# Kernel tuning notes

Measured on AMD Instinct MI355X. Metric: run time of the kernel, lower is better.

## Reference

```python
import jax, jax.numpy as jnp
import numpy as np

EMBED_DIM = 1024
NUM_HEADS = 16
DEPTH = 12
HEAD_DIM = EMBED_DIM // NUM_HEADS // 2  # 32
LAMBDA_INIT = float(0.8 - 0.6 * np.exp(-0.3 * DEPTH))
B, T = 2, 2048


def setup_inputs() -> dict:
    key = jax.random.key(0)
    ks = jax.random.split(key, 10)
    s = 0.02
    return {
        "query": jax.random.normal(ks[0], (B, T, EMBED_DIM), jnp.float32),
        "Wq": jax.random.normal(ks[1], (EMBED_DIM, EMBED_DIM), jnp.float32) * s,
        "Wk": jax.random.normal(ks[2], (EMBED_DIM, EMBED_DIM), jnp.float32) * s,
        "Wv": jax.random.normal(ks[3], (EMBED_DIM, EMBED_DIM), jnp.float32) * s,
        "Wo": jax.random.normal(ks[4], (EMBED_DIM, EMBED_DIM), jnp.float32) * s,
        "lambda_q1": jax.random.normal(ks[5], (HEAD_DIM,), jnp.float32) * 0.1,
        "lambda_k1": jax.random.normal(ks[6], (HEAD_DIM,), jnp.float32) * 0.1,
        "lambda_q2": jax.random.normal(ks[7], (HEAD_DIM,), jnp.float32) * 0.1,
        "lambda_k2": jax.random.normal(ks[8], (HEAD_DIM,), jnp.float32) * 0.1,
        "subln_w": jnp.ones((2 * HEAD_DIM,), jnp.float32),
    }


def reference(query, Wq, Wk, Wv, Wo, lambda_q1, lambda_k1, lambda_q2, lambda_k2, subln_w):
    Bsz, Tt, E = query.shape
    H, hd = NUM_HEADS, HEAD_DIM
    scaling = hd ** -0.5
    # projections (torch Linear: x @ W.T), W stored [out, in]
    q = jnp.einsum('bte,fe->btf', query, Wq).reshape(Bsz, Tt, 2 * H, hd).transpose(0, 2, 1, 3)
    k = jnp.einsum('bse,fe->bsf', query, Wk).reshape(Bsz, Tt, 2 * H, hd).transpose(0, 2, 1, 3)
    v = jnp.einsum('bse,fe->bsf', query, Wv).reshape(Bsz, Tt, H, 2 * hd).transpose(0, 2, 1, 3)
    q = q * scaling
    # dual attention map [B, 2H, T, T], softmax in fp32
    scores = jnp.einsum('bhtd,bhsd->bhts', q, k)
    attn_w = jax.nn.softmax(scores.astype(jnp.float32), axis=-1).astype(q.dtype)
    # learned lambda
    lam1 = jnp.exp(jnp.sum(lambda_q1 * lambda_k1))
    lam2 = jnp.exp(jnp.sum(lambda_q2 * lambda_k2))
    lam = lam1 - lam2 + LAMBDA_INIT
    aw = attn_w.reshape(Bsz, H, 2, Tt, Tt)
    aw = aw[:, :, 0] - lam * aw[:, :, 1]  # [B, H, T, T]
    attn = jnp.einsum('bhts,bhsd->bhtd', aw, v)  # [B, H, T, 2*hd]
    # RMSNorm over last dim (fp32), eps=1e-5, elementwise affine
    x32 = attn.astype(jnp.float32)
    normed = (x32 * jax.lax.rsqrt(jnp.mean(x32 * x32, axis=-1, keepdims=True) + 1e-5)).astype(attn.dtype)
    attn = normed * subln_w
    attn = attn * (1.0 - LAMBDA_INIT)
    out = attn.transpose(0, 2, 1, 3).reshape(Bsz, Tt, H * 2 * hd)
    return jnp.einsum('bte,fe->btf', out, Wo)
```

## Files before the change

### kernel.cpp

```cpp
#include <hip/hip_runtime.h>

typedef short bf16x8 __attribute__((ext_vector_type(8)));
typedef float f32x4 __attribute__((ext_vector_type(4)));
typedef float f32x16 __attribute__((ext_vector_type(16)));
typedef unsigned short ushort_t;
typedef unsigned int uint32;

#define LAMBDA_INIT 0.7836057665316245f
#define TT 2048
#define EE 1024

__device__ __forceinline__ ushort_t f2bf(float x) {
  uint32 b = __float_as_uint(x);
  b += 0x7fffu + ((b >> 16) & 1u);
  return (ushort_t)(b >> 16);
}

__device__ __forceinline__ uint32 cvtpk(float lo, float hi) {
  uint32 r;
  asm("v_cvt_pk_bf16_f32 %0, %1, %2" : "=v"(r) : "v"(lo), "v"(hi));
  return r;
}

__device__ __forceinline__ float fexp2(float x) {
#if __has_builtin(__builtin_amdgcn_exp2f)
  return __builtin_amdgcn_exp2f(x);
#else
  return exp2f(x);
#endif
}

__device__ __forceinline__ bf16x8 mkfrag(uint32 a, uint32 b, uint32 c, uint32 d) {
  union { uint32 w[4]; bf16x8 v; } u;
  u.w[0] = a; u.w[1] = b; u.w[2] = c; u.w[3] = d;
  return u.v;
}

__device__ __forceinline__ void gload16(const void* g, void* l) {
  __builtin_amdgcn_global_load_lds(
      (const __attribute__((address_space(1))) uint32*)g,
      (__attribute__((address_space(3))) uint32*)l, 16, 0, 0);
}

__global__ __launch_bounds__(256) void cvt_all(const float* __restrict__ X,
                                               const float* __restrict__ Wq,
                                               const float* __restrict__ Wk,
                                               const float* __restrict__ Wv,
                                               const float* __restrict__ Wo,
                                               ushort_t* __restrict__ out) {
  const int i = blockIdx.x * 256 + threadIdx.x;
  const float* src;
  int off;
  if (i < 1048576)      { src = X;  off = 0; }
  else if (i < 1310720) { src = Wq; off = 1048576; }
  else if (i < 1572864) { src = Wk; off = 1310720; }
  else if (i < 1835008) { src = Wv; off = 1572864; }
  else                  { src = Wo; off = 1835008; }
  const float4 v = reinterpret_cast<const float4*>(src)[i - off];
  ushort4 o;
  o.x = f2bf(v.x); o.y = f2bf(v.y); o.z = f2bf(v.z); o.w = f2bf(v.w);
  reinterpret_cast<ushort4*>(out)[i] = o;
}

__global__ __launch_bounds__(256) void gemm_bt(const ushort_t* __restrict__ A,
                                               const ushort_t* __restrict__ B,
                                               float* __restrict__ C,
                                               int M, int N, int K, float scale) {
  __shared__ ushort_t As[128 * 32];
  __shared__ ushort_t Bs[128 * 32];
  const int tid = threadIdx.x;
  const int lane = tid & 63, wid = tid >> 6;
  const int wr = wid >> 1, wc = wid & 1;
  const int r16 = lane & 15, g = lane >> 4;
  const int m0 = blockIdx.x * 128, n0 = blockIdx.y * 128;
  f32x4 acc[4][4] = {};
  for (int k0 = 0; k0 < K; k0 += 32) {
#pragma unroll
    for (int c = 0; c < 2; ++c) {
      int eo = wid * 1024 + c * 512 + lane * 8;
      int row = eo >> 5, col = eo & 31;
      gload16(A + (size_t)(m0 + row) * K + k0 + col, As + wid * 1024 + c * 512);
      gload16(B + (size_t)(n0 + row) * K + k0 + col, Bs + wid * 1024 + c * 512);
    }
    __syncthreads();
    bf16x8 af[4], bfg[4];
#pragma unroll
    for (int m = 0; m < 4; ++m)
      af[m] = *reinterpret_cast<const bf16x8*>(As + (wr * 64 + m * 16 + r16) * 32 + g * 8);
#pragma unroll
    for (int n = 0; n < 4; ++n)
      bfg[n] = *reinterpret_cast<const bf16x8*>(Bs + (wc * 64 + n * 16 + r16) * 32 + g * 8);
#pragma unroll
    for (int m = 0; m < 4; ++m)
#pragma unroll
      for (int n = 0; n < 4; ++n)
        acc[m][n] = __builtin_amdgcn_mfma_f32_16x16x32_bf16(af[m], bfg[n], acc[m][n], 0, 0, 0);
    __syncthreads();
  }
#pragma unroll
  for (int m = 0; m < 4; ++m)
#pragma unroll
    for (int n = 0; n < 4; ++n)
#pragma unroll
      for (int r = 0; r < 4; ++r) {
        int row = m0 + wr * 64 + m * 16 + g * 4 + r;
        int col = n0 + wc * 64 + n * 16 + r16;
        C[(size_t)row * N + col] = acc[m][n][r] * scale;
      }
}

#define SHALF(Sbase, Gbase)                                                  \
  do {                                                                       \
    _Pragma("unroll") for (int j_ = 0; j_ < 2; ++j_) {                       \
      const int c_ = wid * 2 + j_;                                           \
      gload16((Gbase) + (size_t)(c_ * 8 + (lane >> 3)) * EE +                \
                  (((lane & 7) ^ (lane >> 3)) << 3),                         \
              (Sbase) + c_ * 512);                                           \
    }                                                                        \
  } while (0)

#define CHUNK(mp)                                                            \
  do {                                                                       \
    __builtin_amdgcn_s_setprio(1);                                           \
    _Pragma("unroll") for (int mm_ = 0; mm_ < 2; ++mm_) {                    \
      const int m_ = (mp) * 2 + mm_;                                         \
      _Pragma("unroll") for (int n_ = 0; n_ < 4; ++n_) {                     \
        acc[m_][n_] = __builtin_amdgcn_mfma_f32_16x16x32_bf16(               \
            af[m_][0], bfr[n_][0], acc[m_][n_], 0, 0, 0);                    \
        acc[m_][n_] = __builtin_amdgcn_mfma_f32_16x16x32_bf16(               \
            af[m_][1], bfr[n_][1], acc[m_][n_], 0, 0, 0);                    \
      }                                                                      \
    }                                                                        \
    __builtin_amdgcn_s_setprio(0);                                           \
  } while (0)

__global__ __launch_bounds__(512, 2) void qkv_gemm256(const ushort_t* __restrict__ A,
                                                      const ushort_t* __restrict__ B,
                                                      ushort_t* __restrict__ C,
                                                      float scale) {
  __shared__ ushort_t Asm[2][16384];
  __shared__ ushort_t Bsm[2][16384];
  const int NKT = EE / 64;
  const int tid = threadIdx.x, lane = tid & 63, wid = tid >> 6;
  const int wr = wid >> 2, wc = wid & 3;
  const int r16 = lane & 15, g = lane >> 4;
  const int w = (blockIdx.x & 7) * 24 + (blockIdx.x >> 3);
  const int bx = w & 15, by = w >> 4;
  const int m0 = bx * 256, n0 = by * 256;
  const ushort_t* Ab = A + (size_t)m0 * EE;
  const ushort_t* Bb = B + (size_t)n0 * EE;

#pragma unroll
  for (int kt = 0; kt < 2; ++kt) {
    SHALF(Asm[kt], Ab + kt * 64);
    SHALF(Asm[kt] + 8192, Ab + (size_t)128 * EE + kt * 64);
    SHALF(Bsm[kt], Bb + kt * 64);
    SHALF(Bsm[kt] + 8192, Bb + (size_t)128 * EE + kt * 64);
  }

  f32x4 acc[8][4] = {};
  for (int t = 0; t < NKT; ++t) {
    const int b = t & 1;
    if (t < NKT - 1) asm volatile("s_waitcnt vmcnt(8)" ::: "memory");
    else             asm volatile("s_waitcnt vmcnt(0)" ::: "memory");
    __builtin_amdgcn_s_barrier();
    asm volatile("" ::: "memory");
    bf16x8 af[8][2], bfr[4][2];
#pragma unroll
    for (int m = 0; m < 8; ++m) {
      const int row = wr * 128 + m * 16 + r16;
#pragma unroll
      for (int kk = 0; kk < 2; ++kk)
        af[m][kk] = *reinterpret_cast<const bf16x8*>(
            Asm[b] + row * 64 + (((kk * 4 + g) ^ (r16 & 7)) << 3));
    }
#pragma unroll
    for (int n = 0; n < 4; ++n) {
      const int row = wc * 64 + n * 16 + r16;
#pragma unroll
      for (int kk = 0; kk < 2; ++kk)
        bfr[n][kk] = *reinterpret_cast<const bf16x8*>(
            Bsm[b] + row * 64 + (((kk * 4 + g) ^ (r16 & 7)) << 3));
    }
    asm volatile("s_waitcnt lgkmcnt(0)" ::: "memory");
    __builtin_amdgcn_s_barrier();
    asm volatile("" ::: "memory");
    const int ts = t + 2;
    const bool st = ts < NKT;
    if (st) SHALF(Asm[b], Ab + ts * 64);
    CHUNK(0);
    if (st) SHALF(Asm[b] + 8192, Ab + (size_t)128 * EE + ts * 64);
    CHUNK(1);
    if (st) SHALF(Bsm[b], Bb + ts * 64);
    CHUNK(2);
    if (st) SHALF(Bsm[b] + 8192, Bb + (size_t)128 * EE + ts * 64);
    CHUNK(3);
  }

  const size_t MN = (size_t)4096 * EE;
#pragma unroll
  for (int m = 0; m < 8; ++m)
#pragma unroll
    for (int n = 0; n < 4; ++n) {
      const int col = n0 + wc * 64 + n * 16 + r16;
      const int seg = col >> 10;
      const int cl = col & 1023;
      if (seg == 2) {
        int row0 = m0 + wr * 128 + m * 16 + g * 4;
        int bb2 = row0 >> 11, t0v = row0 & (TT - 1);
        ushort4 pk;
        pk.x = f2bf(acc[m][n][0]); pk.y = f2bf(acc[m][n][1]);
        pk.z = f2bf(acc[m][n][2]); pk.w = f2bf(acc[m][n][3]);
        *reinterpret_cast<ushort4*>(
            C + 2 * MN + ((size_t)(bb2 * 16 + (cl >> 6)) * 64 + (cl & 63)) * TT + t0v) = pk;
      } else {
        const float sc = (seg == 0) ? scale : 1.0f;
        const size_t base = (size_t)seg * MN;
#pragma unroll
        for (int r = 0; r < 4; ++r) {
          int row = m0 + wr * 128 + m * 16 + g * 4 + r;
          C[base + (size_t)row * EE + cl] = f2bf(acc[m][n][r] * sc);
        }
      }
    }
}

#define PHALF(sv, lacc, oT0, oT1, vf)                                                   \
  do {                                                                                  \
    float p_[16];                                                                       \
    _Pragma("unroll") for (int i_ = 0; i_ < 16; ++i_) p_[i_] = fexp2(sv[i_]);           \
    lacc += (((p_[0] + p_[1]) + (p_[2] + p_[3])) + ((p_[4] + p_[5]) + (p_[6] + p_[7]))) \
          + (((p_[8] + p_[9]) + (p_[10] + p_[11])) +                                    \
             ((p_[12] + p_[13]) + (p_[14] + p_[15])));                                  \
    auto wA_ = __builtin_amdgcn_permlane32_swap((int)cvtpk(p_[0], p_[1]),               \
                                                (int)cvtpk(p_[4], p_[5]), false, false);\
    auto wB_ = __builtin_amdgcn_permlane32_swap((int)cvtpk(p_[2], p_[3]),               \
                                                (int)cvtpk(p_[6], p_[7]), false, false);\
    auto wC_ = __builtin_amdgcn_permlane32_swap((int)cvtpk(p_[8], p_[9]),               \
                                                (int)cvtpk(p_[12], p_[13]), false, false);\
    auto wD_ = __builtin_amdgcn_permlane32_swap((int)cvtpk(p_[10], p_[11]),             \
                                                (int)cvtpk(p_[14], p_[15]), false, false);\
    bf16x8 pa0_ = mkfrag(wA_[0], wB_[0], wA_[1], wB_[1]);                               \
    bf16x8 pa1_ = mkfrag(wC_[0], wD_[0], wC_[1], wD_[1]);                               \
    oT0 = __builtin_amdgcn_mfma_f32_32x32x16_bf16(pa0_, vf[0][0], oT0, 0, 0, 0);        \
    oT0 = __builtin_amdgcn_mfma_f32_32x32x16_bf16(pa1_, vf[1][0], oT0, 0, 0, 0);        \
    oT1 = __builtin_amdgcn_mfma_f32_32x32x16_bf16(pa0_, vf[0][1], oT1, 0, 0, 0);        \
    oT1 = __builtin_amdgcn_mfma_f32_32x32x16_bf16(pa1_, vf[1][1], oT1, 0, 0, 0);        \
  } while (0)

#define STAGE(bi, kv0)                                                                  \
  do {                                                                                  \
    const int r8_ = lane >> 3;                                                          \
    const int g_ = (lane & 7) ^ r8_;                                                    \
    _Pragma("unroll") for (int c2_ = 0; c2_ < 2; ++c2_) {                               \
      const int c_ = wid * 2 + c2_;                                                     \
      gload16(Kg + (size_t)((kv0) + c_ * 8 + r8_) * EE + g_ * 8,                        \
              Ksm[bi] + c_ * 512);                                                      \
      gload16(Vg + (size_t)(c_ * 8 + r8_) * TT + (kv0) + g_ * 8,                        \
              Vsm[bi] + c_ * 512);                                                      \
    }                                                                                   \
  } while (0)

__global__ __launch_bounds__(256, 2) void attn_fused(
    const ushort_t* __restrict__ Q, const ushort_t* __restrict__ K,
    const ushort_t* __restrict__ Vt,
    const float* __restrict__ lq1, const float* __restrict__ lk1,
    const float* __restrict__ lq2, const float* __restrict__ lk2,
    const float* __restrict__ w, ushort_t* __restrict__ X2) {
  __shared__ ushort_t Ksm[2][64 * 64];
  __shared__ ushort_t Vsm[2][64 * 64];
  const int tid = threadIdx.x, lane = tid & 63, wid = tid >> 6;
  const int l31 = lane & 31, hh = lane >> 5;
  const int bid = blockIdx.x;
  const int slice = (bid & 7) + 8 * (bid >> 7);
  const int qb = (bid >> 3) & 15;
  const int bb = slice >> 4, h = slice & 15;
  const int q0 = qb * 128 + wid * 32;

  float prod = (lane < 32) ? lq1[l31] * lk1[l31] : lq2[l31] * lk2[l31];
#pragma unroll
  for (int off = 1; off < 32; off <<= 1) prod += __shfl_xor(prod, off, 32);
  const float lam = __expf(__shfl(prod, 0, 64)) - __expf(__shfl(prod, 32, 64)) + LAMBDA_INIT;

  const ushort_t* Qp = Q + (size_t)(bb * TT + q0 + l31) * EE + h * 64 + hh * 8;
  const bf16x8 qf00 = *reinterpret_cast<const bf16x8*>(Qp);
  const bf16x8 qf01 = *reinterpret_cast<const bf16x8*>(Qp + 16);
  const bf16x8 qf10 = *reinterpret_cast<const bf16x8*>(Qp + 32);
  const bf16x8 qf11 = *reinterpret_cast<const bf16x8*>(Qp + 48);

  const ushort_t* Kg = K + (size_t)bb * TT * EE + h * 64;
  const ushort_t* Vg = Vt + (size_t)(bb * 16 + h) * 64 * TT;
  const int swz = (l31 & 7) << 3;

  f32x16 o00 = {}, o01 = {}, o10 = {}, o11 = {};
  float l0 = 0.f, l1 = 0.f;

  STAGE(0, 0);
  for (int it = 0; it < TT / 64; ++it) {
    const int cur = it & 1;
    __syncthreads();
    if (it + 1 < TT / 64) STAGE(cur ^ 1, (it + 1) * 64);

    const ushort_t* Kt_ = Ksm[cur];
    const ushort_t* Vt_ = Vsm[cur];
#pragma unroll
    for (int s = 0; s < 2; ++s) {
      bf16x8 kf[2][2], vf[2][2];
#pragma unroll
      for (int hf = 0; hf < 2; ++hf)
#pragma unroll
        for (int ks = 0; ks < 2; ++ks)
          kf[hf][ks] = *reinterpret_cast<const bf16x8*>(
              Kt_ + (s * 32 + l31) * 64 + ((hf * 32 + ks * 16 + hh * 8) ^ swz));
#pragma unroll
      for (int ks = 0; ks < 2; ++ks)
#pragma unroll
        for (int dc = 0; dc < 2; ++dc)
          vf[ks][dc] = *reinterpret_cast<const bf16x8*>(
              Vt_ + (dc * 32 + l31) * 64 + ((s * 32 + ks * 16 + hh * 8) ^ swz));

      __builtin_amdgcn_s_setprio(1);
      const f32x16 zz = {};
      f32x16 s0_ = __builtin_amdgcn_mfma_f32_32x32x16_bf16(kf[0][0], qf00, zz, 0, 0, 0);
      s0_ = __builtin_amdgcn_mfma_f32_32x32x16_bf16(kf[0][1], qf01, s0_, 0, 0, 0);
      f32x16 s1_ = __builtin_amdgcn_mfma_f32_32x32x16_bf16(kf[1][0], qf10, zz, 0, 0, 0);
      s1_ = __builtin_amdgcn_mfma_f32_32x32x16_bf16(kf[1][1], qf11, s1_, 0, 0, 0);
      __builtin_amdgcn_s_setprio(0);
      PHALF(s0_, l0, o00, o01, vf);
      PHALF(s1_, l1, o10, o11, vf);
    }
  }

  {
    auto t0 = __builtin_amdgcn_permlane32_swap(__float_as_int(l0), __float_as_int(l0),
                                               false, false);
    l0 = __int_as_float(t0[0]) + __int_as_float(t0[1]);
    auto t1 = __builtin_amdgcn_permlane32_swap(__float_as_int(l1), __float_as_int(l1),
                                               false, false);
    l1 = __int_as_float(t1[0]) + __int_as_float(t1[1]);
  }

  const float w0v = w[l31];
  const float w1v = w[32 + l31];
#pragma unroll
  for (int r = 0; r < 16; ++r) {
    const int qrel = (r & 3) + 8 * (r >> 2) + 4 * hh;
    const float il0 = 1.0f / __shfl(l0, qrel, 64);
    const float il1 = lam / __shfl(l1, qrel, 64);
    const float x0 = o00[r] * il0 - o10[r] * il1;
    const float x1 = o01[r] * il0 - o11[r] * il1;
    float ss = x0 * x0 + x1 * x1;
#pragma unroll
    for (int off = 1; off < 32; off <<= 1) ss += __shfl_xor(ss, off, 64);
    const float sc = rsqrtf(ss * (1.0f / 64.0f) + 1e-5f) * (1.0f - LAMBDA_INIT);
    const size_t ob = (size_t)(bb * TT + q0 + qrel) * EE + h * 64 + l31;
    X2[ob] = f2bf(x0 * sc * w0v);
    X2[ob + 32] = f2bf(x1 * sc * w1v);
  }
}

extern "C" void kernel_launch(void* const* d_in, const int* in_sizes, int n_in,
                              void* d_out, int out_size, void* d_ws, size_t ws_size,
                              hipStream_t stream) {
  const float* X = (const float*)d_in[0];
  const float* Wq = (const float*)d_in[1];
  const float* Wk = (const float*)d_in[2];
  const float* Wv = (const float*)d_in[3];
  const float* Wo = (const float*)d_in[4];
  const float* lq1 = (const float*)d_in[5];
  const float* lk1 = (const float*)d_in[6];
  const float* lq2 = (const float*)d_in[7];
  const float* lk2 = (const float*)d_in[8];
  const float* slw = (const float*)d_in[9];

  const int M = 4096, E = EE;

  ushort_t* Xb = (ushort_t*)d_ws;
  ushort_t* Wqb = Xb + (size_t)M * E;
  ushort_t* Wob = Wqb + (size_t)3 * E * E;
  ushort_t* Qb = Wob + (size_t)E * E;
  ushort_t* Kb = Qb + (size_t)M * E;
  ushort_t* Vtb = Kb + (size_t)M * E;
  ushort_t* X2 = Vtb + (size_t)M * E;

  cvt_all<<<8192, 256, 0, stream>>>(X, Wq, Wk, Wv, Wo, Xb);

  qkv_gemm256<<<192, 512, 0, stream>>>(Xb, Wqb, Qb,
                                       0.17677669529663687f * 1.4426950408889634f);

  attn_fused<<<512, 256, 0, stream>>>(Qb, Kb, Vtb, lq1, lk1, lq2, lk2, slw, X2);

  gemm_bt<<<dim3(M / 128, E / 128), 256, 0, stream>>>(X2, Wob, (float*)d_out, M, E, E,
                                                      1.0f);
}
```

Measured before the change: 137.3 us.

## Split attention KV range across two wave groups and reduce partials in LDS

```diff
diff --git a/kernel.cpp b/kernel.cpp
--- a/kernel.cpp
+++ b/kernel.cpp
@@ -224,6 +224,7 @@
       }
     }
 }
+
 
 #define PHALF(sv, lacc, oT0, oT1, vf)                                                   \
   do {                                                                                  \
@@ -253,29 +254,29 @@
     const int r8_ = lane >> 3;                                                          \
     const int g_ = (lane & 7) ^ r8_;                                                    \
     _Pragma("unroll") for (int c2_ = 0; c2_ < 2; ++c2_) {                               \
-      const int c_ = wid * 2 + c2_;                                                     \
-      gload16(Kg + (size_t)((kv0) + c_ * 8 + r8_) * EE + g_ * 8,                        \
-              Ksm[bi] + c_ * 512);                                                      \
-      gload16(Vg + (size_t)(c_ * 8 + r8_) * TT + (kv0) + g_ * 8,                        \
-              Vsm[bi] + c_ * 512);                                                      \
+      const int c_ = wsub * 2 + c2_;                                                    \
+      gload16(Kgh + (size_t)((kv0) + c_ * 8 + r8_) * EE + g_ * 8,                       \
+              Ksp[bi] + c_ * 512);                                                      \
+      gload16(Vgh + (size_t)(c_ * 8 + r8_) * TT + (kv0) + g_ * 8,                       \
+              Vsp[bi] + c_ * 512);                                                      \
     }                                                                                   \
   } while (0)
 
-__global__ __launch_bounds__(256, 2) void attn_fused(
+__global__ __launch_bounds__(512, 2) void attn_fused(
     const ushort_t* __restrict__ Q, const ushort_t* __restrict__ K,
     const ushort_t* __restrict__ Vt,
     const float* __restrict__ lq1, const float* __restrict__ lk1,
     const float* __restrict__ lq2, const float* __restrict__ lk2,
     const float* __restrict__ w, ushort_t* __restrict__ X2) {
-  __shared__ ushort_t Ksm[2][64 * 64];
-  __shared__ ushort_t Vsm[2][64 * 64];
+  __shared__ ushort_t SMEM[32768];
   const int tid = threadIdx.x, lane = tid & 63, wid = tid >> 6;
+  const int wsub = wid & 3, kvh = wid >> 2;
   const int l31 = lane & 31, hh = lane >> 5;
   const int bid = blockIdx.x;
   const int slice = (bid & 7) + 8 * (bid >> 7);
   const int qb = (bid >> 3) & 15;
   const int bb = slice >> 4, h = slice & 15;
-  const int q0 = qb * 128 + wid * 32;
+  const int q0 = qb * 128 + wsub * 32;
 
   float prod = (lane < 32) ? lq1[l31] * lk1[l31] : lq2[l31] * lk2[l31];
 #pragma unroll
@@ -288,21 +289,24 @@
   const bf16x8 qf10 = *reinterpret_cast<const bf16x8*>(Qp + 32);
   const bf16x8 qf11 = *reinterpret_cast<const bf16x8*>(Qp + 48);
 
-  const ushort_t* Kg = K + (size_t)bb * TT * EE + h * 64;
-  const ushort_t* Vg = Vt + (size_t)(bb * 16 + h) * 64 * TT;
+  const ushort_t* Kgh = K + (size_t)bb * TT * EE + h * 64 + (size_t)(kvh * 1024) * EE;
+  const ushort_t* Vgh = Vt + (size_t)(bb * 16 + h) * 64 * TT + kvh * 1024;
+  ushort_t* const Ksp[2] = {SMEM + (kvh * 2) * 4096, SMEM + (kvh * 2 + 1) * 4096};
+  ushort_t* const Vsp[2] = {SMEM + 16384 + (kvh * 2) * 4096,
+                            SMEM + 16384 + (kvh * 2 + 1) * 4096};
   const int swz = (l31 & 7) << 3;
 
   f32x16 o00 = {}, o01 = {}, o10 = {}, o11 = {};
   float l0 = 0.f, l1 = 0.f;
 
   STAGE(0, 0);
-  for (int it = 0; it < TT / 64; ++it) {
+  for (int it = 0; it < 16; ++it) {
     const int cur = it & 1;
     __syncthreads();
-    if (it + 1 < TT / 64) STAGE(cur ^ 1, (it + 1) * 64);
-
-    const ushort_t* Kt_ = Ksm[cur];
-    const ushort_t* Vt_ = Vsm[cur];
+    if (it + 1 < 16) STAGE(cur ^ 1, (it + 1) * 64);
+
+    const ushort_t* Kt_ = Ksp[cur];
+    const ushort_t* Vt_ = Vsp[cur];
 #pragma unroll
     for (int s = 0; s < 2; ++s) {
       bf16x8 kf[2][2], vf[2][2];
@@ -331,31 +335,69 @@
     }
   }
 
-  {
+  float* scr = (float*)SMEM;
+  __syncthreads();
+  if (wid >= 4) {
+    const int pw = wid - 4;
+#pragma unroll
+    for (int r = 0; r < 16; ++r) {
+      scr[((pw * 2 + 0) * 16 + r) * 64 + lane] = o00[r];
+      scr[((pw * 2 + 1) * 16 + r) * 64 + lane] = o01[r];
+    }
+    scr[8192 + pw * 64 + lane] = l0;
+  }
+  __syncthreads();
+  if (wid < 4) {
+#pragma unroll
+    for (int r = 0; r < 16; ++r) {
+      o00[r] += scr[((wid * 2 + 0) * 16 + r) * 64 + lane];
+      o01[r] += scr[((wid * 2 + 1) * 16 + r) * 64 + lane];
+    }
+    l0 += scr[8192 + wid * 64 + lane];
+  }
+  __syncthreads();
+  if (wid >= 4) {
+    const int pw = wid - 4;
+#pragma unroll
+    for (int r = 0; r < 16; ++r) {
+      scr[((pw * 2 + 0) * 16 + r) * 64 + lane] = o10[r];
+      scr[((pw * 2 + 1) * 16 + r) * 64 + lane] = o11[r];
+    }
+    scr[8192 + pw * 64 + lane] = l1;
+  }
+  __syncthreads();
+  if (wid < 4) {
+#pragma unroll
+    for (int r = 0; r < 16; ++r) {
+      o10[r] += scr[((wid * 2 + 0) * 16 + r) * 64 + lane];
+      o11[r] += scr[((wid * 2 + 1) * 16 + r) * 64 + lane];
+    }
+    l1 += scr[8192 + wid * 64 + lane];
+
     auto t0 = __builtin_amdgcn_permlane32_swap(__float_as_int(l0), __float_as_int(l0),
                                                false, false);
     l0 = __int_as_float(t0[0]) + __int_as_float(t0[1]);
     auto t1 = __builtin_amdgcn_permlane32_swap(__float_as_int(l1), __float_as_int(l1),
                                                false, false);
     l1 = __int_as_float(t1[0]) + __int_as_float(t1[1]);
-  }
-
-  const float w0v = w[l31];
-  const float w1v = w[32 + l31];
-#pragma unroll
-  for (int r = 0; r < 16; ++r) {
-    const int qrel = (r & 3) + 8 * (r >> 2) + 4 * hh;
-    const float il0 = 1.0f / __shfl(l0, qrel, 64);
-    const float il1 = lam / __shfl(l1, qrel, 64);
-    const float x0 = o00[r] * il0 - o10[r] * il1;
-    const float x1 = o01[r] * il0 - o11[r] * il1;
-    float ss = x0 * x0 + x1 * x1;
-#pragma unroll
-    for (int off = 1; off < 32; off <<= 1) ss += __shfl_xor(ss, off, 64);
-    const float sc = rsqrtf(ss * (1.0f / 64.0f) + 1e-5f) * (1.0f - LAMBDA_INIT);
-    const size_t ob = (size_t)(bb * TT + q0 + qrel) * EE + h * 64 + l31;
-    X2[ob] = f2bf(x0 * sc * w0v);
-    X2[ob + 32] = f2bf(x1 * sc * w1v);
+
+    const float w0v = w[l31];
+    const float w1v = w[32 + l31];
+#pragma unroll
+    for (int r = 0; r < 16; ++r) {
+      const int qrel = (r & 3) + 8 * (r >> 2) + 4 * hh;
+      const float il0 = 1.0f / __shfl(l0, qrel, 64);
+      const float il1 = lam / __shfl(l1, qrel, 64);
+      const float x0 = o00[r] * il0 - o10[r] * il1;
+      const float x1 = o01[r] * il0 - o11[r] * il1;
+      float ss = x0 * x0 + x1 * x1;
+#pragma unroll
+      for (int off = 1; off < 32; off <<= 1) ss += __shfl_xor(ss, off, 64);
+      const float sc = rsqrtf(ss * (1.0f / 64.0f) + 1e-5f) * (1.0f - LAMBDA_INIT);
+      const size_t ob = (size_t)(bb * TT + q0 + qrel) * EE + h * 64 + l31;
+      X2[ob] = f2bf(x0 * sc * w0v);
+      X2[ob + 32] = f2bf(x1 * sc * w1v);
+    }
   }
 }
 
@@ -388,7 +430,7 @@
   qkv_gemm256<<<192, 512, 0, stream>>>(Xb, Wqb, Qb,
                                        0.17677669529663687f * 1.4426950408889634f);
 
-  attn_fused<<<512, 256, 0, stream>>>(Qb, Kb, Vtb, lq1, lk1, lq2, lk2, slw, X2);
+  attn_fused<<<512, 512, 0, stream>>>(Qb, Kb, Vtb, lq1, lk1, lq2, lk2, slw, X2);
 
   gemm_bt<<<dim3(M / 128, E / 128), 256, 0, stream>>>(X2, Wob, (float*)d_out, M, E, E,
                                                       1.0f);
```

Result: slower. 150.7 us (+9.7%).
